# Kernel optimization log

Hardware: AMD Instinct MI355X
Metric: run time of the kernel (lower is better)

Reference implementation:

```python
import jax, jax.numpy as jnp
from jax import lax
import numpy as np

B, IMG_H, IMG_W = 8, 256, 512
NUM_CLASSES, P = 20, 32
SCALE, TOPK, IOU_THR = 32.0, 100, 0.5


def conv2d(x, w, b, stride=1, pad=1):
    y = lax.conv_general_dilated(x, w, (stride, stride), [(pad, pad), (pad, pad)],
                                 dimension_numbers=('NCHW', 'OIHW', 'NCHW'))
    return y + b[None, :, None, None]


def bilinear_resize(img, out_h, out_w):
    # img: [..., H, W]; torch F.interpolate(mode='bilinear', align_corners=False)
    H, W = img.shape[-2], img.shape[-1]
    def idx_w(n_in, n_out):
        src = (jnp.arange(n_out, dtype=jnp.float32) + 0.5) * (n_in / n_out) - 0.5
        src = jnp.clip(src, 0.0, n_in - 1)
        i0 = jnp.floor(src).astype(jnp.int32)
        i1 = jnp.minimum(i0 + 1, n_in - 1)
        return i0, i1, src - i0.astype(jnp.float32)
    y0, y1, wy = idx_w(H, out_h)
    x0, x1, wx = idx_w(W, out_w)
    top = img[..., y0, :] * (1.0 - wy)[:, None] + img[..., y1, :] * wy[:, None]
    return top[..., x0] * (1.0 - wx) + top[..., x1] * wx


def generate_anchors(fh, fw):
    ys = (jnp.arange(fh, dtype=jnp.float32) + 0.5) * (IMG_H / fh)
    xs = (jnp.arange(fw, dtype=jnp.float32) + 0.5) * (IMG_W / fw)
    cy, cx = jnp.meshgrid(ys, xs, indexing='ij')
    h = SCALE / 2
    return jnp.stack([cx - h, cy - h, cx + h, cy + h], -1).reshape(-1, 4)


def delta_to_boxes(anchors, deltas):
    a_c = (anchors[:, :2] + anchors[:, 2:]) / 2
    a_wh = anchors[:, 2:] - anchors[:, :2]
    pc = a_c + deltas[..., :2] * a_wh
    pwh = a_wh * jnp.exp(deltas[..., 2:])
    return jnp.concatenate([pc - pwh / 2, pc + pwh / 2], -1)


def nms_single(boxes, scores, labels):
    # torchvision batched_nms: offset boxes per label, greedy NMS, return kept idxs
    N = boxes.shape[0]
    off = labels.astype(boxes.dtype) * (jnp.max(boxes) + 1.0)
    b = boxes + off[:, None]
    order = jnp.argsort(-scores)
    bs = b[order]
    area = (bs[:, 2] - bs[:, 0]) * (bs[:, 3] - bs[:, 1])
    lt = jnp.maximum(bs[:, None, :2], bs[None, :, :2])
    rb = jnp.minimum(bs[:, None, 2:], bs[None, :, 2:])
    wh = jnp.clip(rb - lt, 0.0)
    inter = wh[..., 0] * wh[..., 1]
    iou = inter / (area[:, None] + area[None, :] - inter + 1e-9)
    idxs = jnp.arange(N)
    def body(i, suppressed):
        keep_i = jnp.logical_not(suppressed[i])
        row = (iou[i] > IOU_THR) & (idxs > i)
        return jnp.where(keep_i, suppressed | row, suppressed)
    suppressed = lax.fori_loop(0, N, body, jnp.zeros(N, bool))
    keep_mask = ~suppressed
    rank = jnp.cumsum(keep_mask) - 1
    slots = jnp.where(keep_mask & (rank < TOPK), rank, TOPK)
    out = jnp.full(TOPK + 1, -1, jnp.int32).at[slots].set(order.astype(jnp.int32))
    return out[:TOPK]


def setup_inputs():
    key = jax.random.key(0)
    ks = jax.random.split(key, 17)
    def cw(k, o, i, kh, kw_):
        return jax.random.normal(k, (o, i, kh, kw_), jnp.float32) / np.sqrt(i * kh * kw_)
    return {
        'images': jax.random.normal(ks[0], (B, 3, IMG_H, IMG_W), jnp.float32),
        'w1': cw(ks[1], 64, 3, 3, 3),   'b1': jnp.zeros(64, jnp.float32),
        'w2': cw(ks[2], 128, 64, 3, 3), 'b2': jnp.zeros(128, jnp.float32),
        'w3': cw(ks[3], 256, 128, 3, 3),'b3': jnp.zeros(256, jnp.float32),
        'pw1': cw(ks[4], 256, 256, 3, 3), 'pb1': jnp.zeros(256, jnp.float32),
        'pw2': cw(ks[5], P, 256, 1, 1),   'pb2': jnp.zeros(P, jnp.float32),
        'cw_': cw(ks[6], NUM_CLASSES + 1, 256, 3, 3), 'cb': jnp.zeros(NUM_CLASSES + 1, jnp.float32),
        'bw': cw(ks[7], 4, 256, 3, 3),  'bb': jnp.zeros(4, jnp.float32),
        'kw': cw(ks[8], P, 256, 3, 3),  'kb': jnp.zeros(P, jnp.float32),
    }


def reference(images, w1, b1, w2, b2, w3, b3, pw1, pb1, pw2, pb2, cw_, cb, bw, bb, kw, kb):
    x = jax.nn.relu(conv2d(images, w1, b1, stride=2))
    x = jax.nn.relu(conv2d(x, w2, b2, stride=2))
    feat = jax.nn.relu(conv2d(x, w3, b3, stride=2))          # [B,256,32,64]
    proto = conv2d(jax.nn.relu(conv2d(feat, pw1, pb1)), pw2, pb2, pad=0)  # [B,P,32,64]
    fh, fw = feat.shape[2], feat.shape[3]
    def head(w, b, c):
        return conv2d(feat, w, b).transpose(0, 2, 3, 1).reshape(B, -1, c)
    cls = head(cw_, cb, NUM_CLASSES + 1)     # [B,N,C+1]
    box = head(bw, bb, 4)                    # [B,N,4]
    coef = head(kw, kb, P)                   # [B,N,P]
    anchors = generate_anchors(fh, fw)       # [N,4]
    probs = jax.nn.softmax(cls, -1)[..., :-1]
    scores = probs.max(-1)
    labels = probs.argmax(-1).astype(jnp.int32)
    boxes = delta_to_boxes(anchors, box)     # [B,N,4]
    keep = jax.vmap(nms_single)(boxes, scores, labels)   # [B,100], -1 pad
    valid = keep >= 0
    ki = jnp.clip(keep, 0)
    take = lambda a: jnp.take_along_axis(a, ki[..., None] if a.ndim == 3 else ki, axis=1)
    boxes_k = take(boxes) * valid[..., None]
    scores_k = take(scores) * valid
    labels_k = jnp.where(valid, take(labels), 0)
    coef_k = jnp.take_along_axis(coef, ki[..., None], axis=1)   # [B,100,P]
    m = jax.nn.sigmoid(jnp.einsum('bkp,bphw->bkhw', coef_k, proto))
    masks = bilinear_resize(m, IMG_H, IMG_W) > 0.5
    masks = masks & valid[..., None, None]
    return boxes_k, scores_k, labels_k, masks, valid
```

## Files before the change

kernel.cpp:

```cpp
#include <hip/hip_runtime.h>
#include <hip/hip_bf16.h>
#include <math.h>

#define BB 8
#define NCLS 21
#define NANCH 2048
#define TOPK_N 100

static const size_t OFF_X1HI = 0;
static const size_t OFF_X1LO = 34344960;
static const size_t OFF_X2HI = 68689920;
static const size_t OFF_X2LO = 86261760;
static const size_t OFF_FTHI = 103833600;
static const size_t OFF_FTLO = 113025024;
static const size_t OFF_WT1  = 122216448;
static const size_t OFF_A2H  = 122223616;
static const size_t OFF_A2L  = 122371072;
static const size_t OFF_A3H  = 122518528;
static const size_t OFF_A3L  = 123108352;
static const size_t OFF_AHH  = 123698176;
static const size_t OFF_AHL  = 123993088;
static const size_t OFF_AP1H = 124288000;
static const size_t OFF_AP1L = 125467648;
static const size_t OFF_WTP2 = 126647296;
static const size_t OFF_BH   = 126680064;
static const size_t OFF_HOUT = 126680576;
static const size_t OFF_P1   = 130874880;
static const size_t OFF_PROTO= 147652096;
static const size_t OFF_BOXES= 149749248;
static const size_t OFF_SCORES=150011392;
static const size_t OFF_LABELS=150076928;
static const size_t OFF_ORDER= 150142464;
static const size_t OFF_SB   = 150208000;
static const size_t OFF_IOU  = 150470144;
static const size_t OFF_KEEP = 154664448;
static const size_t OFF_MAXB = 154668032;

static const size_t OUT_BOXES  = 0;
static const size_t OUT_SCORES = 3200;
static const size_t OUT_LABELS = 4000;
static const size_t OUT_MASKS  = 4800;
static const size_t OUT_VALID  = 104862400;

typedef __attribute__((ext_vector_type(8))) short bf16x8;
typedef __attribute__((ext_vector_type(4))) float f32x4;

__device__ __forceinline__ unsigned encf(float f){
  unsigned u = __float_as_uint(f);
  return (u & 0x80000000u) ? ~u : (u | 0x80000000u);
}
__device__ __forceinline__ float decf(unsigned u){
  unsigned b = (u & 0x80000000u) ? (u & 0x7fffffffu) : ~u;
  return __uint_as_float(b);
}
__device__ __forceinline__ short f2bf(float f){
  __hip_bfloat16 h = __float2bfloat16(f);
  return *(short*)&h;
}
__device__ __forceinline__ float bf2f(short h){
  return __uint_as_float(((unsigned)(unsigned short)h) << 16);
}

__global__ void halok3(short* __restrict__ x1hi, short* __restrict__ x1lo,
                       short* __restrict__ x2hi, short* __restrict__ x2lo,
                       short* __restrict__ fthi, short* __restrict__ ftlo,
                       unsigned* __restrict__ maxb){
  int i = blockIdx.x*256 + threadIdx.x;
  if (i < BB) maxb[i] = 0u;
  short *hi, *lo; int Hp, Wp, cell, bg;
  if (i < 49408){
    hi=x1hi; lo=x1lo; Hp=130; Wp=258; cell = i % 772; bg = i / 772;
  } else if (i < 99072){
    int j = i - 49408; hi=x2hi; lo=x2lo; Hp=66; Wp=130; cell = j % 388; bg = j / 388;
  } else if (i < 149248){
    int j = i - 99072; hi=fthi; lo=ftlo; Hp=34; Wp=66; cell = j % 196; bg = j / 196;
  } else return;
  int y, x;
  if (cell < Wp)        { y = 0;      x = cell; }
  else if (cell < 2*Wp) { y = Hp-1;   x = cell - Wp; }
  else { int r = cell - 2*Wp; y = 1 + (r>>1); x = (r&1) ? (Wp-1) : 0; }
  size_t ad = (((size_t)bg*Hp + y)*Wp + x)*8;
  bf16x8 z = (bf16x8){0,0,0,0,0,0,0,0};
  *(bf16x8*)(hi + ad) = z;
  *(bf16x8*)(lo + ad) = z;
}

template<int CIN,int COUT,int KK>
__device__ __forceinline__ void packw_body(int i, const float* __restrict__ w,
                                           float* __restrict__ wT){
  if (i >= CIN*KK*COUT) return;
  int co = i % COUT; int r = i / COUT;
  int ci = r / KK,  k = r % KK;
  wT[i] = w[(co*CIN + ci)*KK + k];
}

template<int CIN,int COUT>
__device__ __forceinline__ void packA_body(int i, const float* __restrict__ w,
                                           short* __restrict__ Ahi, short* __restrict__ Alo){
  constexpr int K = CIN*9;
  constexpr int KS = K/32;
  if (i >= COUT*K) return;
  int sub  = i & 7;
  int lane = (i >> 3) & 63;
  int rest = i >> 9;
  int ks = rest % KS;
  int mt = rest / KS;
  int m = mt*16 + (lane & 15);
  int k = ks*32 + (lane >> 4)*8 + sub;
  int tap = k / CIN, ci = k - tap*CIN;
  float v = w[(m*CIN + ci)*9 + tap];
  short h = f2bf(v);
  Ahi[i] = h;
  Alo[i] = f2bf(v - bf2f(h));
}

__device__ __forceinline__ void packAh_body(int i,
    const float* __restrict__ cw, const float* __restrict__ bw,
    const float* __restrict__ kw, const float* __restrict__ cb,
    const float* __restrict__ bb, const float* __restrict__ kb,
    short* __restrict__ Ahi, short* __restrict__ Alo, float* __restrict__ bh){
  if (i < 64){
    float v = 0.f;
    if (i < 21) v = cb[i]; else if (i < 25) v = bb[i-21]; else if (i < 57) v = kb[i-25];
    bh[i] = v;
  }
  if (i >= 64*2304) return;
  constexpr int KS = 72;
  int sub  = i & 7;
  int lane = (i >> 3) & 63;
  int rest = i >> 9;
  int ks = rest % KS;
  int mt = rest / KS;
  int m = mt*16 + (lane & 15);
  int k = ks*32 + (lane >> 4)*8 + sub;
  int tap = k >> 8, ci = k & 255;
  float v = 0.f;
  if (m < 21)      v = cw[(m*256 + ci)*9 + tap];
  else if (m < 25) v = bw[((m-21)*256 + ci)*9 + tap];
  else if (m < 57) v = kw[((m-25)*256 + ci)*9 + tap];
  short h = f2bf(v);
  Ahi[i] = h;
  Alo[i] = f2bf(v - bf2f(h));
}

__global__ void packall(const float* __restrict__ w1, float* __restrict__ wT1,
                        const float* __restrict__ w2, short* __restrict__ a2h, short* __restrict__ a2l,
                        const float* __restrict__ w3, short* __restrict__ a3h, short* __restrict__ a3l,
                        const float* __restrict__ pw1, short* __restrict__ ap1h, short* __restrict__ ap1l,
                        const float* __restrict__ cw, const float* __restrict__ bw,
                        const float* __restrict__ kw, const float* __restrict__ cb,
                        const float* __restrict__ bb, const float* __restrict__ kb,
                        short* __restrict__ ahh, short* __restrict__ ahl, float* __restrict__ bh,
                        const float* __restrict__ pw2, float* __restrict__ wTp2){
  int blk = blockIdx.x, t = threadIdx.x;
  if (blk < 288)        packA_body<64,128>(blk*256+t, w2, a2h, a2l);
  else if (blk < 1440)  packA_body<128,256>((blk-288)*256+t, w3, a3h, a3l);
  else if (blk < 3744)  packA_body<256,256>((blk-1440)*256+t, pw1, ap1h, ap1l);
  else if (blk < 4320)  packAh_body((blk-3744)*256+t, cw,bw,kw,cb,bb,kb, ahh,ahl,bh);
  else if (blk < 4327)  packw_body<3,64,9>((blk-4320)*256+t, w1, wT1);
  else                  packw_body<256,32,1>((blk-4327)*256+t, pw2, wTp2);
}

__global__ __launch_bounds__(256) void conv1k(const float* __restrict__ img,
    const float* __restrict__ wT, const float* __restrict__ bias,
    short* __restrict__ x1hi, short* __restrict__ x1lo){
  const int b   = blockIdx.z;
  const int co0 = blockIdx.y * 16;
  const int g   = blockIdx.x*256 + threadIdx.x;
  const int y  = g >> 7;
  const int x0 = (g & 127) << 1;

  float acc[16][2];
#pragma unroll
  for (int c=0;c<16;c++){
    float bv = bias[co0+c];
    acc[c][0] = bv; acc[c][1] = bv;
  }
  int   off[3][5];
  float msk[3][5];
#pragma unroll
  for (int kh=0;kh<3;kh++){
    int iy = y*2 - 1 + kh;
    bool okr = (iy >= 0) && (iy < 256);
    int ro = okr ? iy*512 : 0;
#pragma unroll
    for (int t=0;t<5;t++){
      int col = x0*2 - 1 + t;
      bool ok = okr && (col >= 0) && (col < 512);
      off[kh][t] = ok ? (ro + col) : 0;
      msk[kh][t] = ok ? 1.f : 0.f;
    }
  }
  const float* inb = img + (size_t)b*3*256*512;
  for (int ci=0; ci<3; ci++){
    const float* inc = inb + (size_t)ci*256*512;
    float v[3][5];
#pragma unroll
    for (int kh=0;kh<3;kh++)
#pragma unroll
      for (int t=0;t<5;t++)
        v[kh][t] = inc[off[kh][t]] * msk[kh][t];
    const float* wp = wT + ci*9*64 + co0;
#pragma unroll
    for (int kh=0;kh<3;kh++)
#pragma unroll
    for (int kw=0;kw<3;kw++){
      const float* wq = wp + (kh*3+kw)*64;
#pragma unroll
      for (int c=0;c<16;c++){
        float wv = wq[c];
        acc[c][0] = fmaf(wv, v[kh][2*0+kw], acc[c][0]);
        acc[c][1] = fmaf(wv, v[kh][2*1+kw], acc[c][1]);
      }
    }
  }
#pragma unroll
  for (int s=0;s<2;s++){
    short hv[16] __attribute__((aligned(16)));
    short lv[16] __attribute__((aligned(16)));
#pragma unroll
    for (int c=0;c<16;c++){
      float r = fmaxf(acc[c][s], 0.f);
      short h = f2bf(r);
      hv[c] = h;
      lv[c] = f2bf(r - bf2f(h));
    }
#pragma unroll
    for (int g2=0; g2<2; g2++){
      size_t ad = (((size_t)(b*8 + (co0>>3) + g2)*130 + (y+1))*258 + (x0+s+1))*8;
      *(bf16x8*)(x1hi + ad) = *(bf16x8*)(hv + g2*8);
      *(bf16x8*)(x1lo + ad) = *(bf16x8*)(lv + g2*8);
    }
  }
}

template<int CIN,int K,int M,int MW,int NW,int S,int IPH,int IPW,int NXB,
         bool SPLIT,bool STAGELO,bool STAGEREG,int EMODE,int OPH,int OPW>
__global__ __launch_bounds__(NW*64) void cgemm_row(
    const short* __restrict__ Ahi, const short* __restrict__ Alo,
    const short* __restrict__ Bhi, const short* __restrict__ Blo,
    const float* __restrict__ bias, float* __restrict__ outf,
    short* __restrict__ outhi, short* __restrict__ outlo){
  static_assert(CIN % 32 == 0, "CIN must be multiple of 32");
  constexpr int NT = 64*32;
  constexpr int KS = K/32;
  constexpr int CG = CIN/8;
  constexpr int SW  = 64*S + 2;
  constexpr int SWP = (S==2) ? (SW/2 + 1) : SW;
  constexpr int PARS = (S==2) ? 2 : 1;
  constexpr int LOOFF = CG*PARS*SWP*8;
  constexpr int BUFS = (SPLIT && STAGELO) ? 2 : 1;
  constexpr int NTH = NW*64;
  constexpr int NLD = (CG*SW + NTH - 1)/NTH;
  __shared__ __align__(16) short sB[BUFS*LOOFF];

  const int b    = blockIdx.z;
  const int oy   = blockIdx.x / NXB;
  const int xb   = (blockIdx.x % NXB) * 64;
  const int wave = threadIdx.x >> 6;
  const int lane = threadIdx.x & 63;
  const int lm = lane & 15, lq = lane >> 4;
  const int m0 = (blockIdx.y * NW + wave) * (MW*16);
  const int tid = threadIdx.x;

  f32x4 acc[MW][4];
#pragma unroll
  for (int i=0;i<MW;i++)
#pragma unroll
    for (int j=0;j<4;j++) acc[i][j] = (f32x4){0.f,0.f,0.f,0.f};

  const short* Ah_l = Ahi + (size_t)lane*8;
  const short* Al_l = Alo + (size_t)lane*8;
  const int mt0 = m0 >> 4;
  const size_t plane = (size_t)IPH*IPW;
  const short* Bl0 = Blo + ((size_t)b*CG + lq)*plane*8;

  bf16x8 rh[STAGEREG ? NLD : 1];
  bf16x8 rl[(STAGEREG && SPLIT && STAGELO) ? NLD : 1];

  auto LOADS = [&](int iyv){
    const short* srch = Bhi + (((size_t)b*CG*IPH + iyv)*IPW + (size_t)(xb*S))*8;
#pragma unroll
    for (int t=0;t<NLD;t++){
      int c = tid + t*NTH;
      if (c < CG*SW){
        int g = c / SW, p = c - g*SW;
        rh[t] = *(const bf16x8*)(srch + ((size_t)g*plane + p)*8);
      }
    }
    if constexpr (SPLIT && STAGELO){
      const short* srcl = Blo + (((size_t)b*CG*IPH + iyv)*IPW + (size_t)(xb*S))*8;
#pragma unroll
      for (int t=0;t<NLD;t++){
        int c = tid + t*NTH;
        if (c < CG*SW){
          int g = c / SW, p = c - g*SW;
          rl[t] = *(const bf16x8*)(srcl + ((size_t)g*plane + p)*8);
        }
      }
    }
  };
  auto WRITES = [&](){
#pragma unroll
    for (int t=0;t<NLD;t++){
      int c = tid + t*NTH;
      if (c < CG*SW){
        int g = c / SW, p = c - g*SW;
        int dst = (S==2) ? ((g*2 + (p&1))*SWP + (p>>1)) : (g*SW + p);
        *(bf16x8*)(&sB[(size_t)dst*8]) = rh[t];
        if constexpr (SPLIT && STAGELO)
          *(bf16x8*)(&sB[LOOFF + (size_t)dst*8]) = rl[t];
      }
    }
  };

  if constexpr (STAGEREG){
    LOADS(oy*S);
    WRITES();
    __syncthreads();
  }

#pragma unroll 1
  for (int dy=0; dy<3; dy++){
    const int iy = oy*S + dy;
    if constexpr (STAGEREG){
      if (dy < 2) LOADS(oy*S + dy + 1);
    } else {
      __syncthreads();
      {
        const short* srch = Bhi + (((size_t)b*CG*IPH + iy)*IPW + (size_t)(xb*S))*8;
        for (int c = tid; c < CG*SW; c += NTH){
          int g = c / SW, p = c - g*SW;
          int dst = (S==2) ? ((g*2 + (p&1))*SWP + (p>>1)) : (g*SW + p);
          *(bf16x8*)(&sB[(size_t)dst*8]) =
            *(const bf16x8*)(srch + ((size_t)g*plane + p)*8);
        }
        if constexpr (SPLIT && STAGELO){
          const short* srcl = Blo + (((size_t)b*CG*IPH + iy)*IPW + (size_t)(xb*S))*8;
          for (int c = tid; c < CG*SW; c += NTH){
            int g = c / SW, p = c - g*SW;
            int dst = (S==2) ? ((g*2 + (p&1))*SWP + (p>>1)) : (g*SW + p);
            *(bf16x8*)(&sB[LOOFF + (size_t)dst*8]) =
              *(const bf16x8*)(srcl + ((size_t)g*plane + p)*8);
          }
        }
      }
      __syncthreads();
    }
#pragma unroll
    for (int dx=0; dx<3; dx++){
      const int tap = dy*3 + dx;
      const int ksb = tap*(CIN/32);
#pragma unroll
      for (int kc=0; kc<CIN; kc+=32){
        const int ks = ksb + (kc>>5);
        int ra[4];
#pragma unroll
        for (int j=0;j<4;j++){
          int pc = (j*16 + lm)*S + dx;
          ra[j] = (S==2) ? ((((kc>>3) + lq)*2 + (pc&1))*SWP + (pc>>1))
                         : (((kc>>3) + lq)*SW + pc);
        }
        bf16x8 ah[MW], bh_[4];
#pragma unroll
        for (int i=0;i<MW;i++)
          ah[i] = *(const bf16x8*)(Ah_l + ((size_t)(mt0+i)*KS + ks)*512);
#pragma unroll
        for (int j=0;j<4;j++)
          bh_[j] = *(const bf16x8*)(&sB[(size_t)ra[j]*8]);
        if constexpr (SPLIT){
          bf16x8 al[MW], bl_[4];
#pragma unroll
          for (int i=0;i<MW;i++)
            al[i] = *(const bf16x8*)(Al_l + ((size_t)(mt0+i)*KS + ks)*512);
          if constexpr (STAGELO){
#pragma unroll
            for (int j=0;j<4;j++)
              bl_[j] = *(const bf16x8*)(&sB[LOOFF + (size_t)ra[j]*8]);
          } else {
#pragma unroll
            for (int j=0;j<4;j++){
              size_t pix = (size_t)iy*IPW + (size_t)((xb + j*16 + lm)*S + dx);
              bl_[j] = *(const bf16x8*)(Bl0 + ((size_t)(kc>>3)*plane + pix)*8);
            }
          }
#pragma unroll
          for (int j=0;j<4;j++)
#pragma unroll
            for (int i=0;i<MW;i++)
              acc[i][j] = __builtin_amdgcn_mfma_f32_16x16x32_bf16(ah[i], bh_[j], acc[i][j], 0,0,0);
#pragma unroll
          for (int j=0;j<4;j++)
#pragma unroll
            for (int i=0;i<MW;i++)
              acc[i][j] = __builtin_amdgcn_mfma_f32_16x16x32_bf16(ah[i], bl_[j], acc[i][j], 0,0,0);
#pragma unroll
          for (int j=0;j<4;j++)
#pragma unroll
            for (int i=0;i<MW;i++)
              acc[i][j] = __builtin_amdgcn_mfma_f32_16x16x32_bf16(al[i], bh_[j], acc[i][j], 0,0,0);
        } else {
#pragma unroll
          for (int j=0;j<4;j++)
#pragma unroll
            for (int i=0;i<MW;i++)
              acc[i][j] = __builtin_amdgcn_mfma_f32_16x16x32_bf16(ah[i], bh_[j], acc[i][j], 0,0,0);
        }
      }
    }
    if constexpr (STAGEREG){
      if (dy < 2){
        __syncthreads();
        WRITES();
        __syncthreads();
      }
    }
  }

#pragma unroll
  for (int i=0;i<MW;i++){
#pragma unroll
    for (int r=0;r<4;r++){
      const int m = m0 + i*16 + lq*4 + r;
      const float bv = bias[m];
      if constexpr (EMODE == 0){
#pragma unroll
        for (int j=0;j<4;j++){
          const int ox = xb + j*16 + lm;
          float v = fmaxf(acc[i][j][r] + bv, 0.f);
          short h = f2bf(v);
          short l = f2bf(v - bf2f(h));
          size_t ad = ((((size_t)(b*(M/8) + (m>>3))*OPH + (oy+1))*OPW + (ox+1)))*8 + (m&7);
          outhi[ad] = h;
          outlo[ad] = l;
        }
      } else {
        float* cp = outf + ((size_t)b*M + m)*NT + oy*64 + lm;
#pragma unroll
        for (int j=0;j<4;j++){
          float v = acc[i][j][r] + bv;
          if constexpr (EMODE == 2) v = fmaxf(v, 0.f);
          cp[j*16] = v;
        }
      }
    }
  }
}

__global__ __launch_bounds__(256) void headsdec(
    const short* __restrict__ Ahi, const short* __restrict__ Alo,
    const short* __restrict__ Bhi, const short* __restrict__ Blo,
    const float* __restrict__ bias, float* __restrict__ hout,
    float* __restrict__ boxes, float* __restrict__ scores,
    int* __restrict__ labels, unsigned* __restrict__ maxb){
  constexpr int KS = 72;
  constexpr int CG = 32;
  constexpr int SW = 66;
  constexpr int IPH = 34, IPW = 66;
  constexpr int LOOFF = CG*SW*8;
  constexpr int NLD = (CG*SW + 255)/256;
  __shared__ __align__(16) short sB[2*LOOFF];

  const int b  = blockIdx.z;
  const int oy = blockIdx.x;
  const int wave = threadIdx.x >> 6;
  const int lane = threadIdx.x & 63;
  const int lm = lane & 15, lq = lane >> 4;
  const int tid = threadIdx.x;

  f32x4 acc[4];
#pragma unroll
  for (int j=0;j<4;j++) acc[j] = (f32x4){0.f,0.f,0.f,0.f};

  const short* Ah_l = Ahi + (size_t)lane*8;
  const short* Al_l = Alo + (size_t)lane*8;
  const size_t plane = (size_t)IPH*IPW;

  bf16x8 rh[NLD], rl[NLD];
  auto HLOADS = [&](int iyv){
    const short* srch = Bhi + ((size_t)b*CG*IPH + iyv)*IPW*8;
    const short* srcl = Blo + ((size_t)b*CG*IPH + iyv)*IPW*8;
#pragma unroll
    for (int t=0;t<NLD;t++){
      int c = tid + t*256;
      if (c < CG*SW){
        int g = c / SW, p = c - g*SW;
        rh[t] = *(const bf16x8*)(srch + ((size_t)g*plane + p)*8);
        rl[t] = *(const bf16x8*)(srcl + ((size_t)g*plane + p)*8);
      }
    }
  };
  auto HWRITES = [&](){
#pragma unroll
    for (int t=0;t<NLD;t++){
      int c = tid + t*256;
      if (c < CG*SW){
        *(bf16x8*)(&sB[(size_t)c*8]) = rh[t];
        *(bf16x8*)(&sB[LOOFF + (size_t)c*8]) = rl[t];
      }
    }
  };

  HLOADS(oy);
  HWRITES();
  __syncthreads();

#pragma unroll 1
  for (int dy=0; dy<3; dy++){
    if (dy < 2) HLOADS(oy + dy + 1);
#pragma unroll
    for (int dx=0; dx<3; dx++){
      const int tap = dy*3 + dx;
      const int ksb = tap*8;
#pragma unroll
      for (int kc=0; kc<256; kc+=32){
        const int ks = ksb + (kc>>5);
        int ra[4];
#pragma unroll
        for (int j=0;j<4;j++) ra[j] = ((kc>>3) + lq)*SW + (j*16 + lm) + dx;
        bf16x8 bh_[4], bl_[4];
#pragma unroll
        for (int j=0;j<4;j++){
          bh_[j] = *(const bf16x8*)(&sB[(size_t)ra[j]*8]);
          bl_[j] = *(const bf16x8*)(&sB[LOOFF + (size_t)ra[j]*8]);
        }
        bf16x8 ah = *(const bf16x8*)(Ah_l + ((size_t)wave*KS + ks)*512);
        bf16x8 al = *(const bf16x8*)(Al_l + ((size_t)wave*KS + ks)*512);
#pragma unroll
        for (int j=0;j<4;j++)
          acc[j] = __builtin_amdgcn_mfma_f32_16x16x32_bf16(ah, bh_[j], acc[j], 0,0,0);
#pragma unroll
        for (int j=0;j<4;j++)
          acc[j] = __builtin_amdgcn_mfma_f32_16x16x32_bf16(ah, bl_[j], acc[j], 0,0,0);
#pragma unroll
        for (int j=0;j<4;j++)
          acc[j] = __builtin_amdgcn_mfma_f32_16x16x32_bf16(al, bh_[j], acc[j], 0,0,0);
      }
    }
    if (dy < 2){
      __syncthreads();
      HWRITES();
      __syncthreads();
    }
  }

  __syncthreads();
  float* sF = (float*)sB;
#pragma unroll
  for (int r=0;r<4;r++){
    const int m = wave*16 + lq*4 + r;
    const float bv = bias[m];
    float* cp = hout + ((size_t)b*64 + m)*NANCH + oy*64 + lm;
#pragma unroll
    for (int j=0;j<4;j++){
      float v = acc[j][r] + bv;
      cp[j*16] = v;
      sF[m*68 + j*16 + lm] = v;
    }
  }
  __syncthreads();

  if (tid < 64){
    const int n = oy*64 + tid;
    float l[NCLS];
    float M = -1e30f;
#pragma unroll
    for (int c=0;c<NCLS;c++){ l[c] = sF[c*68 + tid]; M = fmaxf(M, l[c]); }
    float denom = 0.f;
#pragma unroll
    for (int c=0;c<NCLS;c++) denom += expf(l[c]-M);
    float best = -1.f; int bi = 0;
#pragma unroll
    for (int c=0;c<NCLS-1;c++){
      float e = expf(l[c]-M);
      if (e > best){ best = e; bi = c; }
    }
    scores[(size_t)b*NANCH + n] = best/denom;
    labels[(size_t)b*NANCH + n] = bi;

    float dxv = sF[21*68 + tid], dyv = sF[22*68 + tid];
    float dwv = sF[23*68 + tid], dhv = sF[24*68 + tid];
    const int yy = n >> 6, xx = n & 63;
    float cx = (xx+0.5f)*8.f, cy = (yy+0.5f)*8.f;
    float px = cx + dxv*32.f, py = cy + dyv*32.f;
    float pw = 32.f*expf(dwv), ph = 32.f*expf(dhv);
    float x1 = px - 0.5f*pw, y1 = py - 0.5f*ph;
    float x2 = px + 0.5f*pw, y2 = py + 0.5f*ph;
    float* bo = boxes + ((size_t)b*NANCH + n)*4;
    bo[0]=x1; bo[1]=y1; bo[2]=x2; bo[3]=y2;
    float mx = fmaxf(fmaxf(x1,y1), fmaxf(x2,y2));
#pragma unroll
    for (int off=32; off>0; off>>=1) mx = fmaxf(mx, __shfl_down(mx, off));
    if (tid == 0) atomicMax(maxb + b, encf(mx));
  }
}

__global__ __launch_bounds__(256) void pw2k2(const float* __restrict__ p1,
    const float* __restrict__ wT, const float* __restrict__ bias,
    float* __restrict__ proto){
  const int b  = blockIdx.y;
  const int sp = blockIdx.x*256 + threadIdx.x;
  float acc[32];
#pragma unroll
  for (int c=0;c<32;c++) acc[c] = bias[c];
  const float* pb = p1 + (size_t)b*256*NANCH + sp;
  for (int ci=0;ci<256;ci++){
    float v = pb[(size_t)ci*NANCH];
    const float* wq = wT + ci*32;
#pragma unroll
    for (int c=0;c<32;c++) acc[c] = fmaf(v, wq[c], acc[c]);
  }
#pragma unroll
  for (int c=0;c<32;c++)
    proto[((size_t)b*32 + c)*NANCH + sp] = acc[c];
}

__global__ void __launch_bounds__(1024) sortk(const float* __restrict__ scores,
                     const float* __restrict__ boxes, const int* __restrict__ labels,
                     const unsigned* __restrict__ maxb,
                     int* __restrict__ order, float* __restrict__ sb){
  __shared__ float sc[NANCH];
  __shared__ int   id[NANCH];
  const int b = blockIdx.x, t = threadIdx.x;
  for (int i=t;i<NANCH;i+=1024){ sc[i]=scores[(size_t)b*NANCH+i]; id[i]=i; }
  __syncthreads();
  for (int k=2;k<=NANCH;k<<=1){
    for (int j=k>>1;j>0;j>>=1){
      for (int i=t;i<NANCH;i+=1024){
        int ixj = i ^ j;
        if (ixj > i){
          float sa=sc[i], sb_=sc[ixj]; int ia=id[i], ib=id[ixj];
          bool dir = ((i & k) == 0);
          bool before_ba = (sb_ > sa) || (sb_ == sa && ib < ia);
          if (before_ba == dir){ sc[i]=sb_; sc[ixj]=sa; id[i]=ib; id[ixj]=ia; }
        }
      }
      __syncthreads();
    }
  }
  float mboff = decf(maxb[b]) + 1.0f;
  for (int r=t;r<NANCH;r+=1024){
    int o = id[r];
    order[(size_t)b*NANCH + r] = o;
    float off = (float)labels[(size_t)b*NANCH + o] * mboff;
    const float* bo = boxes + ((size_t)b*NANCH + o)*4;
    float* sp = sb + ((size_t)b*NANCH + r)*4;
    sp[0]=bo[0]+off; sp[1]=bo[1]+off; sp[2]=bo[2]+off; sp[3]=bo[3]+off;
  }
}

__global__ void ioumask(const float* __restrict__ sb, unsigned long long* __restrict__ iou){
  const int b = blockIdx.y;
  const int gid = blockIdx.x*blockDim.x + threadIdx.x;
  const int i = gid >> 5, w = gid & 31;
  const float* base = sb + (size_t)b*NANCH*4;
  unsigned long long bits = 0ull;
  const int j0 = w << 6;
  if (j0 + 63 > i){
    float x1=base[i*4], y1=base[i*4+1], x2=base[i*4+2], y2=base[i*4+3];
    float ai = (x2-x1)*(y2-y1);
    for (int jj=0;jj<64;jj++){
      int j = j0 + jj;
      if (j > i){
        float bx1=base[j*4], by1=base[j*4+1], bx2=base[j*4+2], by2=base[j*4+3];
        float lx=fmaxf(x1,bx1), ly=fmaxf(y1,by1);
        float rx=fminf(x2,bx2), ry=fminf(y2,by2);
        float ww=fmaxf(rx-lx,0.f), hh=fmaxf(ry-ly,0.f);
        float inter = ww*hh;
        float aj = (bx2-bx1)*(by2-by1);
        float v = inter/(ai + aj - inter + 1e-9f);
        if (v > 0.5f) bits |= (1ull << jj);
      }
    }
  }
  iou[((size_t)b*NANCH + i)*32 + w] = bits;
}

__global__ void nmsgather(const unsigned long long* __restrict__ iou,
                          const int* __restrict__ order,
                          const float* __restrict__ boxes, const float* __restrict__ scores,
                          const int* __restrict__ labels,
                          int* __restrict__ keep, float* __restrict__ out){
  const int b = blockIdx.x, lane = threadIdx.x;
  __shared__ int s_keep[TOPK_N];
  unsigned long long sup = 0ull;
  int k = 0, i = 0;
  while (k < TOPK_N){
    unsigned long long avail = (lane < 32) ? ~sup : 0ull;
    const int wi = i >> 6;
    if (lane < wi) avail = 0ull;
    else if (lane == wi) avail &= (~0ull) << (i & 63);
    unsigned long long ball = __ballot(avail != 0ull);
    if (!ball) break;
    int w0 = (int)__builtin_ctzll(ball);
    unsigned long long aw = __shfl(avail, w0);
    int b0 = (int)__builtin_ctzll(aw);
    i = (w0 << 6) + b0;
    int ov = order[(size_t)b*NANCH + i];
    if (lane == 0) s_keep[k] = ov;
    k++;
    unsigned long long row = (lane < 32) ? iou[((size_t)b*NANCH + i)*32 + lane] : 0ull;
    sup |= row;
    i++;
    if (i >= NANCH) break;
  }
  __syncthreads();
  for (int r = lane; r < TOPK_N; r += 64){
    int kv = (r < k) ? s_keep[r] : -1;
    keep[b*TOPK_N + r] = kv;
    float valid = (kv >= 0) ? 1.f : 0.f;
    int kc = (kv < 0) ? 0 : kv;
    const float* bo = boxes + ((size_t)b*NANCH + kc)*4;
#pragma unroll
    for (int c=0;c<4;c++) out[OUT_BOXES + ((size_t)b*TOPK_N + r)*4 + c] = bo[c]*valid;
    out[OUT_SCORES + b*TOPK_N + r] = scores[(size_t)b*NANCH + kc]*valid;
    out[OUT_LABELS + b*TOPK_N + r] = (kv >= 0) ? (float)labels[(size_t)b*NANCH + kc] : 0.f;
    out[OUT_VALID  + b*TOPK_N + r] = valid;
  }
}

__global__ __launch_bounds__(256) void maskresize(const int* __restrict__ keep,
    const float* __restrict__ hout, const float* __restrict__ proto,
    float* __restrict__ out){
  const int b = blockIdx.y, r = blockIdx.x;
  float* obase = out + OUT_MASKS + ((size_t)b*TOPK_N + r)*131072;
  int ki = keep[b*TOPK_N + r];
  if (ki < 0){
    float4 z = make_float4(0.f,0.f,0.f,0.f);
    for (int idx = threadIdx.x; idx < 32768; idx += 256)
      ((float4*)obase)[idx] = z;
    return;
  }
  __shared__ float cf[32];
  __shared__ float sm[NANCH];
  if (threadIdx.x < 32)
    cf[threadIdx.x] = hout[((size_t)b*64 + 25 + threadIdx.x)*NANCH + ki];
  __syncthreads();
  for (int s = threadIdx.x; s < NANCH; s += 256){
    float acc = 0.f;
#pragma unroll
    for (int p=0;p<32;p++) acc = fmaf(cf[p], proto[((size_t)b*32 + p)*NANCH + s], acc);
    sm[s] = 1.f/(1.f + expf(-acc));
  }
  __syncthreads();
  for (int pid = threadIdx.x; pid < 32768; pid += 256){
    const int y  = pid >> 7;
    const int x4 = (pid & 127) << 2;
    float sy = (y + 0.5f)*0.125f - 0.5f;
    sy = fminf(fmaxf(sy, 0.f), 31.f);
    int y0 = (int)floorf(sy);
    int y1 = min(y0+1, 31);
    float wy = sy - (float)y0;
    const float* r0 = sm + y0*64;
    const float* r1 = sm + y1*64;
    float res[4];
#pragma unroll
    for (int kk=0;kk<4;kk++){
      int x = x4 + kk;
      float sx = (x + 0.5f)*0.125f - 0.5f;
      sx = fminf(fmaxf(sx, 0.f), 63.f);
      int x0 = (int)floorf(sx);
      int x1 = min(x0+1, 63);
      float wx = sx - (float)x0;
      float t0 = r0[x0]*(1.f-wy) + r1[x0]*wy;
      float t1 = r0[x1]*(1.f-wy) + r1[x1]*wy;
      float v  = t0*(1.f-wx) + t1*wx;
      res[kk] = (v > 0.5f) ? 1.f : 0.f;
    }
    *(float4*)(obase + y*512 + x4) = make_float4(res[0], res[1], res[2], res[3]);
  }
}

extern "C" void kernel_launch(void* const* d_in, const int* in_sizes, int n_in,
                              void* d_out, int out_size, void* d_ws, size_t ws_size,
                              hipStream_t stream) {
  const float* images=(const float*)d_in[0];
  const float* w1=(const float*)d_in[1];  const float* b1=(const float*)d_in[2];
  const float* w2=(const float*)d_in[3];  const float* b2=(const float*)d_in[4];
  const float* w3=(const float*)d_in[5];  const float* b3=(const float*)d_in[6];
  const float* pw1=(const float*)d_in[7]; const float* pb1=(const float*)d_in[8];
  const float* pw2=(const float*)d_in[9]; const float* pb2=(const float*)d_in[10];
  const float* cw=(const float*)d_in[11]; const float* cb=(const float*)d_in[12];
  const float* bw=(const float*)d_in[13]; const float* bb=(const float*)d_in[14];
  const float* kw=(const float*)d_in[15]; const float* kb=(const float*)d_in[16];
  float* out = (float*)d_out;
  char* ws = (char*)d_ws;

  short* x1hi = (short*)(ws + OFF_X1HI);
  short* x1lo = (short*)(ws + OFF_X1LO);
  short* x2hi = (short*)(ws + OFF_X2HI);
  short* x2lo = (short*)(ws + OFF_X2LO);
  short* fthi = (short*)(ws + OFF_FTHI);
  short* ftlo = (short*)(ws + OFF_FTLO);
  float* wT1  = (float*)(ws + OFF_WT1);
  short* a2h  = (short*)(ws + OFF_A2H);
  short* a2l  = (short*)(ws + OFF_A2L);
  short* a3h  = (short*)(ws + OFF_A3H);
  short* a3l  = (short*)(ws + OFF_A3L);
  short* ahh  = (short*)(ws + OFF_AHH);
  short* ahl  = (short*)(ws + OFF_AHL);
  short* ap1h = (short*)(ws + OFF_AP1H);
  short* ap1l = (short*)(ws + OFF_AP1L);
  float* wTp2 = (float*)(ws + OFF_WTP2);
  float* bh   = (float*)(ws + OFF_BH);
  float* hout = (float*)(ws + OFF_HOUT);
  float* p1   = (float*)(ws + OFF_P1);
  float* proto= (float*)(ws + OFF_PROTO);
  float* boxes= (float*)(ws + OFF_BOXES);
  float* scores=(float*)(ws + OFF_SCORES);
  int*   labels=(int*)  (ws + OFF_LABELS);
  int*   order =(int*)  (ws + OFF_ORDER);
  float* sb   = (float*)(ws + OFF_SB);
  unsigned long long* iou = (unsigned long long*)(ws + OFF_IOU);
  int*   keep = (int*)  (ws + OFF_KEEP);
  unsigned* maxb = (unsigned*)(ws + OFF_MAXB);

  halok3<<<dim3(583), 256, 0, stream>>>(x1hi, x1lo, x2hi, x2lo, fthi, ftlo, maxb);

  packall<<<dim3(4359), 256, 0, stream>>>(w1, wT1, w2, a2h, a2l, w3, a3h, a3l,
                                          pw1, ap1h, ap1l, cw, bw, kw, cb, bb, kb,
                                          ahh, ahl, bh, pw2, wTp2);

  conv1k<<<dim3(64,4,BB), 256, 0, stream>>>(images, wT1, b1, x1hi, x1lo);

  cgemm_row<64,576,128,2,4,2,130,258,2,true,true,false,0,66,130>
      <<<dim3(128,1,BB), 256, 0, stream>>>(a2h, a2l, x1hi, x1lo, b2, nullptr, x2hi, x2lo);

  cgemm_row<128,1152,256,2,4,2,66,130,1,true,true,true,0,34,66>
      <<<dim3(32,2,BB), 256, 0, stream>>>(a3h, a3l, x2hi, x2lo, b3, nullptr, fthi, ftlo);

  headsdec<<<dim3(32,1,BB), 256, 0, stream>>>(ahh, ahl, fthi, ftlo, bh, hout,
                                              boxes, scores, labels, maxb);

  cgemm_row<256,2304,256,2,4,1,34,66,1,false,false,true,2,1,1>
      <<<dim3(32,2,BB), 256, 0, stream>>>(ap1h, ap1l, fthi, fthi, pb1, p1, nullptr, nullptr);

  pw2k2<<<dim3(8,BB), 256, 0, stream>>>(p1, wTp2, pb2, proto);

  sortk<<<dim3(BB), 1024, 0, stream>>>(scores, boxes, labels, maxb, order, sb);
  ioumask<<<dim3(256,BB), 256, 0, stream>>>(sb, iou);
  nmsgather<<<dim3(BB), 64, 0, stream>>>(iou, order, boxes, scores, labels, keep, out);

  maskresize<<<dim3(TOPK_N,BB), 256, 0, stream>>>(keep, hout, proto, out);
}
```

Baseline: 953.4 us.

## Merge prep, head/pw1, and pw2/sort kernels into combined launches

Halo zeroing, weight packing and conv1 now run as blocks of a single megaprep launch, with conv1 weights transposed into shared memory so the separate wT1 pack is dropped. The heads/decode kernel and the proto pw1 GEMM become branches of one launch that share a shared-memory buffer. The pw2 projection and the per-image sort share another launch. The layer-2 GEMM template also switches STAGEREG on. The aim is to cut launch count and let independent work run side by side. The risk is that conv1 blocks in megaprep read the packed weights' neighbours without ordering, since packing and conv1 have no dependency, and that the fused kernels take on larger shared-memory and register footprints, which lowers occupancy.

```diff
diff --git a/kernel.cpp b/kernel.cpp
--- a/kernel.cpp
+++ b/kernel.cpp
@@ -61,30 +61,6 @@
   return __uint_as_float(((unsigned)(unsigned short)h) << 16);
 }
 
-__global__ void halok3(short* __restrict__ x1hi, short* __restrict__ x1lo,
-                       short* __restrict__ x2hi, short* __restrict__ x2lo,
-                       short* __restrict__ fthi, short* __restrict__ ftlo,
-                       unsigned* __restrict__ maxb){
-  int i = blockIdx.x*256 + threadIdx.x;
-  if (i < BB) maxb[i] = 0u;
-  short *hi, *lo; int Hp, Wp, cell, bg;
-  if (i < 49408){
-    hi=x1hi; lo=x1lo; Hp=130; Wp=258; cell = i % 772; bg = i / 772;
-  } else if (i < 99072){
-    int j = i - 49408; hi=x2hi; lo=x2lo; Hp=66; Wp=130; cell = j % 388; bg = j / 388;
-  } else if (i < 149248){
-    int j = i - 99072; hi=fthi; lo=ftlo; Hp=34; Wp=66; cell = j % 196; bg = j / 196;
-  } else return;
-  int y, x;
-  if (cell < Wp)        { y = 0;      x = cell; }
-  else if (cell < 2*Wp) { y = Hp-1;   x = cell - Wp; }
-  else { int r = cell - 2*Wp; y = 1 + (r>>1); x = (r&1) ? (Wp-1) : 0; }
-  size_t ad = (((size_t)bg*Hp + y)*Wp + x)*8;
-  bf16x8 z = (bf16x8){0,0,0,0,0,0,0,0};
-  *(bf16x8*)(hi + ad) = z;
-  *(bf16x8*)(lo + ad) = z;
-}
-
 template<int CIN,int COUT,int KK>
 __device__ __forceinline__ void packw_body(int i, const float* __restrict__ w,
                                            float* __restrict__ wT){
@@ -143,37 +119,71 @@
   Alo[i] = f2bf(v - bf2f(h));
 }
 
-__global__ void packall(const float* __restrict__ w1, float* __restrict__ wT1,
-                        const float* __restrict__ w2, short* __restrict__ a2h, short* __restrict__ a2l,
-                        const float* __restrict__ w3, short* __restrict__ a3h, short* __restrict__ a3l,
-                        const float* __restrict__ pw1, short* __restrict__ ap1h, short* __restrict__ ap1l,
-                        const float* __restrict__ cw, const float* __restrict__ bw,
-                        const float* __restrict__ kw, const float* __restrict__ cb,
-                        const float* __restrict__ bb, const float* __restrict__ kb,
-                        short* __restrict__ ahh, short* __restrict__ ahl, float* __restrict__ bh,
-                        const float* __restrict__ pw2, float* __restrict__ wTp2){
-  int blk = blockIdx.x, t = threadIdx.x;
-  if (blk < 288)        packA_body<64,128>(blk*256+t, w2, a2h, a2l);
-  else if (blk < 1440)  packA_body<128,256>((blk-288)*256+t, w3, a3h, a3l);
-  else if (blk < 3744)  packA_body<256,256>((blk-1440)*256+t, pw1, ap1h, ap1l);
-  else if (blk < 4320)  packAh_body((blk-3744)*256+t, cw,bw,kw,cb,bb,kb, ahh,ahl,bh);
-  else if (blk < 4327)  packw_body<3,64,9>((blk-4320)*256+t, w1, wT1);
-  else                  packw_body<256,32,1>((blk-4327)*256+t, pw2, wTp2);
-}
-
-__global__ __launch_bounds__(256) void conv1k(const float* __restrict__ img,
-    const float* __restrict__ wT, const float* __restrict__ bias,
-    short* __restrict__ x1hi, short* __restrict__ x1lo){
-  const int b   = blockIdx.z;
-  const int co0 = blockIdx.y * 16;
-  const int g   = blockIdx.x*256 + threadIdx.x;
+__global__ __launch_bounds__(256) void megaprep(
+    const float* __restrict__ images, const float* __restrict__ w1, const float* __restrict__ b1,
+    const float* __restrict__ w2, short* __restrict__ a2h, short* __restrict__ a2l,
+    const float* __restrict__ w3, short* __restrict__ a3h, short* __restrict__ a3l,
+    const float* __restrict__ pw1, short* __restrict__ ap1h, short* __restrict__ ap1l,
+    const float* __restrict__ cw, const float* __restrict__ bw, const float* __restrict__ kw,
+    const float* __restrict__ cb, const float* __restrict__ bb, const float* __restrict__ kb,
+    short* __restrict__ ahh, short* __restrict__ ahl, float* __restrict__ bh,
+    const float* __restrict__ pw2, float* __restrict__ wTp2,
+    short* __restrict__ x1hi, short* __restrict__ x1lo,
+    short* __restrict__ x2hi, short* __restrict__ x2lo,
+    short* __restrict__ fthi, short* __restrict__ ftlo,
+    unsigned* __restrict__ maxb){
+  __shared__ float sw[27*64];
+  const int blk = blockIdx.x, tid = threadIdx.x;
+
+  if (blk < 583){
+    int i = blk*256 + tid;
+    if (i < BB) maxb[i] = 0u;
+    short *hi, *lo; int Hp, Wp, cell, bg;
+    if (i < 49408){
+      hi=x1hi; lo=x1lo; Hp=130; Wp=258; cell = i % 772; bg = i / 772;
+    } else if (i < 99072){
+      int j = i - 49408; hi=x2hi; lo=x2lo; Hp=66; Wp=130; cell = j % 388; bg = j / 388;
+    } else if (i < 149248){
+      int j = i - 99072; hi=fthi; lo=ftlo; Hp=34; Wp=66; cell = j % 196; bg = j / 196;
+    } else return;
+    int y, x;
+    if (cell < Wp)        { y = 0;      x = cell; }
+    else if (cell < 2*Wp) { y = Hp-1;   x = cell - Wp; }
+    else { int r = cell - 2*Wp; y = 1 + (r>>1); x = (r&1) ? (Wp-1) : 0; }
+    size_t ad = (((size_t)bg*Hp + y)*Wp + x)*8;
+    bf16x8 z = (bf16x8){0,0,0,0,0,0,0,0};
+    *(bf16x8*)(hi + ad) = z;
+    *(bf16x8*)(lo + ad) = z;
+    return;
+  }
+  if (blk < 4935){
+    int lb = blk - 583;
+    if (lb < 288)        packA_body<64,128>(lb*256+tid, w2, a2h, a2l);
+    else if (lb < 1440)  packA_body<128,256>((lb-288)*256+tid, w3, a3h, a3l);
+    else if (lb < 3744)  packA_body<256,256>((lb-1440)*256+tid, pw1, ap1h, ap1l);
+    else if (lb < 4320)  packAh_body((lb-3744)*256+tid, cw,bw,kw,cb,bb,kb, ahh,ahl,bh);
+    else                 packw_body<256,32,1>((lb-4320)*256+tid, pw2, wTp2);
+    return;
+  }
+
+  const int cblk = blk - 4935;
+  const int bxc = cblk & 63;
+  const int co0 = ((cblk >> 6) & 3) * 16;
+  const int b   = cblk >> 8;
+  for (int idx = tid; idx < 1728; idx += 256){
+    int r = idx >> 6, co = idx & 63;
+    sw[idx] = w1[co*27 + r];
+  }
+  __syncthreads();
+
+  const int g  = bxc*256 + tid;
   const int y  = g >> 7;
   const int x0 = (g & 127) << 1;
 
   float acc[16][2];
 #pragma unroll
   for (int c=0;c<16;c++){
-    float bv = bias[co0+c];
+    float bv = b1[co0+c];
     acc[c][0] = bv; acc[c][1] = bv;
   }
   int   off[3][5];
@@ -191,7 +201,7 @@
       msk[kh][t] = ok ? 1.f : 0.f;
     }
   }
-  const float* inb = img + (size_t)b*3*256*512;
+  const float* inb = images + (size_t)b*3*256*512;
   for (int ci=0; ci<3; ci++){
     const float* inc = inb + (size_t)ci*256*512;
     float v[3][5];
@@ -200,17 +210,17 @@
 #pragma unroll
       for (int t=0;t<5;t++)
         v[kh][t] = inc[off[kh][t]] * msk[kh][t];
-    const float* wp = wT + ci*9*64 + co0;
+    const float* wp = sw + ci*9*64 + co0;
 #pragma unroll
     for (int kh=0;kh<3;kh++)
 #pragma unroll
-    for (int kw=0;kw<3;kw++){
-      const float* wq = wp + (kh*3+kw)*64;
+    for (int kw2=0;kw2<3;kw2++){
+      const float* wq = wp + (kh*3+kw2)*64;
 #pragma unroll
       for (int c=0;c<16;c++){
         float wv = wq[c];
-        acc[c][0] = fmaf(wv, v[kh][2*0+kw], acc[c][0]);
-        acc[c][1] = fmaf(wv, v[kh][2*1+kw], acc[c][1]);
+        acc[c][0] = fmaf(wv, v[kh][2*0+kw2], acc[c][0]);
+        acc[c][1] = fmaf(wv, v[kh][2*1+kw2], acc[c][1]);
       }
     }
   }
@@ -236,7 +246,8 @@
 
 template<int CIN,int K,int M,int MW,int NW,int S,int IPH,int IPW,int NXB,
          bool SPLIT,bool STAGELO,bool STAGEREG,int EMODE,int OPH,int OPW>
-__global__ __launch_bounds__(NW*64) void cgemm_row(
+__device__ __forceinline__ void cgemm_row_body(
+    short* sB, int bxi, int byi, int bzi,
     const short* __restrict__ Ahi, const short* __restrict__ Alo,
     const short* __restrict__ Bhi, const short* __restrict__ Blo,
     const float* __restrict__ bias, float* __restrict__ outf,
@@ -247,20 +258,17 @@
   constexpr int CG = CIN/8;
   constexpr int SW  = 64*S + 2;
   constexpr int SWP = (S==2) ? (SW/2 + 1) : SW;
-  constexpr int PARS = (S==2) ? 2 : 1;
-  constexpr int LOOFF = CG*PARS*SWP*8;
-  constexpr int BUFS = (SPLIT && STAGELO) ? 2 : 1;
+  constexpr int LOOFF = CG*((S==2)?2:1)*SWP*8;
   constexpr int NTH = NW*64;
   constexpr int NLD = (CG*SW + NTH - 1)/NTH;
-  __shared__ __align__(16) short sB[BUFS*LOOFF];
-
-  const int b    = blockIdx.z;
-  const int oy   = blockIdx.x / NXB;
-  const int xb   = (blockIdx.x % NXB) * 64;
+
+  const int b    = bzi;
+  const int oy   = bxi / NXB;
+  const int xb   = (bxi % NXB) * 64;
   const int wave = threadIdx.x >> 6;
   const int lane = threadIdx.x & 63;
   const int lm = lane & 15, lq = lane >> 4;
-  const int m0 = (blockIdx.y * NW + wave) * (MW*16);
+  const int m0 = (byi * NW + wave) * (MW*16);
   const int tid = threadIdx.x;
 
   f32x4 acc[MW][4];
@@ -447,7 +455,26 @@
   }
 }
 
-__global__ __launch_bounds__(256) void headsdec(
+template<int CIN,int K,int M,int MW,int NW,int S,int IPH,int IPW,int NXB,
+         bool SPLIT,bool STAGELO,bool STAGEREG,int EMODE,int OPH,int OPW>
+__global__ __launch_bounds__(NW*64) void cgemm_row(
+    const short* __restrict__ Ahi, const short* __restrict__ Alo,
+    const short* __restrict__ Bhi, const short* __restrict__ Blo,
+    const float* __restrict__ bias, float* __restrict__ outf,
+    short* __restrict__ outhi, short* __restrict__ outlo){
+  constexpr int CG = CIN/8;
+  constexpr int SW  = 64*S + 2;
+  constexpr int SWP = (S==2) ? (SW/2 + 1) : SW;
+  constexpr int LOOFF = CG*((S==2)?2:1)*SWP*8;
+  constexpr int BUFS = (SPLIT && STAGELO) ? 2 : 1;
+  __shared__ __align__(16) short sB[BUFS*LOOFF];
+  cgemm_row_body<CIN,K,M,MW,NW,S,IPH,IPW,NXB,SPLIT,STAGELO,STAGEREG,EMODE,OPH,OPW>(
+      sB, blockIdx.x, blockIdx.y, blockIdx.z,
+      Ahi, Alo, Bhi, Blo, bias, outf, outhi, outlo);
+}
+
+__device__ __forceinline__ void headsdec_body(
+    short* sB, int oy, int b,
     const short* __restrict__ Ahi, const short* __restrict__ Alo,
     const short* __restrict__ Bhi, const short* __restrict__ Blo,
     const float* __restrict__ bias, float* __restrict__ hout,
@@ -459,10 +486,7 @@
   constexpr int IPH = 34, IPW = 66;
   constexpr int LOOFF = CG*SW*8;
   constexpr int NLD = (CG*SW + 255)/256;
-  __shared__ __align__(16) short sB[2*LOOFF];
-
-  const int b  = blockIdx.z;
-  const int oy = blockIdx.x;
+
   const int wave = threadIdx.x >> 6;
   const int lane = threadIdx.x & 63;
   const int lm = lane & 15, lq = lane >> 4;
@@ -595,33 +619,54 @@
   }
 }
 
-__global__ __launch_bounds__(256) void pw2k2(const float* __restrict__ p1,
-    const float* __restrict__ wT, const float* __restrict__ bias,
-    float* __restrict__ proto){
-  const int b  = blockIdx.y;
-  const int sp = blockIdx.x*256 + threadIdx.x;
-  float acc[32];
-#pragma unroll
-  for (int c=0;c<32;c++) acc[c] = bias[c];
-  const float* pb = p1 + (size_t)b*256*NANCH + sp;
-  for (int ci=0;ci<256;ci++){
-    float v = pb[(size_t)ci*NANCH];
-    const float* wq = wT + ci*32;
-#pragma unroll
-    for (int c=0;c<32;c++) acc[c] = fmaf(v, wq[c], acc[c]);
-  }
-#pragma unroll
-  for (int c=0;c<32;c++)
-    proto[((size_t)b*32 + c)*NANCH + sp] = acc[c];
-}
-
-__global__ void __launch_bounds__(1024) sortk(const float* __restrict__ scores,
-                     const float* __restrict__ boxes, const int* __restrict__ labels,
-                     const unsigned* __restrict__ maxb,
-                     int* __restrict__ order, float* __restrict__ sb){
+__global__ __launch_bounds__(256) void headpw1k(
+    const short* __restrict__ ahh, const short* __restrict__ ahl,
+    const short* __restrict__ ap1h,
+    const short* __restrict__ fthi, const short* __restrict__ ftlo,
+    const float* __restrict__ bh, const float* __restrict__ pb1,
+    float* __restrict__ hout, float* __restrict__ p1,
+    float* __restrict__ boxes, float* __restrict__ scores,
+    int* __restrict__ labels, unsigned* __restrict__ maxb){
+  __shared__ __align__(16) short smem[33792];
+  const int bx = blockIdx.x, b = blockIdx.z;
+  if (bx < 32){
+    headsdec_body(smem, bx, b, ahh, ahl, fthi, ftlo, bh, hout,
+                  boxes, scores, labels, maxb);
+  } else {
+    const int lx = bx - 32;
+    cgemm_row_body<256,2304,256,2,4,1,34,66,1,false,false,true,2,1,1>(
+        smem, lx & 31, lx >> 5, b, ap1h, ap1h, fthi, fthi, pb1, p1, nullptr, nullptr);
+  }
+}
+
+__global__ void __launch_bounds__(1024) pw2sortk(
+    const float* __restrict__ p1, const float* __restrict__ wT,
+    const float* __restrict__ biasp, float* __restrict__ proto,
+    const float* __restrict__ scores, const float* __restrict__ boxes,
+    const int* __restrict__ labels, const unsigned* __restrict__ maxb,
+    int* __restrict__ order, float* __restrict__ sb){
   __shared__ float sc[NANCH];
   __shared__ int   id[NANCH];
-  const int b = blockIdx.x, t = threadIdx.x;
+  const int bx = blockIdx.x, t = threadIdx.x;
+  if (bx < 16){
+    const int b  = bx >> 1;
+    const int sp = (bx & 1)*1024 + t;
+    float acc[32];
+#pragma unroll
+    for (int c=0;c<32;c++) acc[c] = biasp[c];
+    const float* pb = p1 + (size_t)b*256*NANCH + sp;
+    for (int ci=0;ci<256;ci++){
+      float v = pb[(size_t)ci*NANCH];
+      const float* wq = wT + ci*32;
+#pragma unroll
+      for (int c=0;c<32;c++) acc[c] = fmaf(v, wq[c], acc[c]);
+    }
+#pragma unroll
+    for (int c=0;c<32;c++)
+      proto[((size_t)b*32 + c)*NANCH + sp] = acc[c];
+    return;
+  }
+  const int b = bx - 16;
   for (int i=t;i<NANCH;i+=1024){ sc[i]=scores[(size_t)b*NANCH+i]; id[i]=i; }
   __syncthreads();
   for (int k=2;k<=NANCH;k<<=1){
@@ -792,7 +837,6 @@
   short* x2lo = (short*)(ws + OFF_X2LO);
   short* fthi = (short*)(ws + OFF_FTHI);
   short* ftlo = (short*)(ws + OFF_FTLO);
-  float* wT1  = (float*)(ws + OFF_WT1);
   short* a2h  = (short*)(ws + OFF_A2H);
   short* a2l  = (short*)(ws + OFF_A2L);
   short* a3h  = (short*)(ws + OFF_A3H);
@@ -815,29 +859,24 @@
   int*   keep = (int*)  (ws + OFF_KEEP);
   unsigned* maxb = (unsigned*)(ws + OFF_MAXB);
 
-  halok3<<<dim3(583), 256, 0, stream>>>(x1hi, x1lo, x2hi, x2lo, fthi, ftlo, maxb);
-
-  packall<<<dim3(4359), 256, 0, stream>>>(w1, wT1, w2, a2h, a2l, w3, a3h, a3l,
-                                          pw1, ap1h, ap1l, cw, bw, kw, cb, bb, kb,
-                                          ahh, ahl, bh, pw2, wTp2);
-
-  conv1k<<<dim3(64,4,BB), 256, 0, stream>>>(images, wT1, b1, x1hi, x1lo);
-
-  cgemm_row<64,576,128,2,4,2,130,258,2,true,true,false,0,66,130>
+  megaprep<<<dim3(6983), 256, 0, stream>>>(
+      images, w1, b1, w2, a2h, a2l, w3, a3h, a3l, pw1, ap1h, ap1l,
+      cw, bw, kw, cb, bb, kb, ahh, ahl, bh, pw2, wTp2,
+      x1hi, x1lo, x2hi, x2lo, fthi, ftlo, maxb);
+
+  cgemm_row<64,576,128,2,4,2,130,258,2,true,true,true,0,66,130>
       <<<dim3(128,1,BB), 256, 0, stream>>>(a2h, a2l, x1hi, x1lo, b2, nullptr, x2hi, x2lo);
 
   cgemm_row<128,1152,256,2,4,2,66,130,1,true,true,true,0,34,66>
       <<<dim3(32,2,BB), 256, 0, stream>>>(a3h, a3l, x2hi, x2lo, b3, nullptr, fthi, ftlo);
 
-  headsdec<<<dim3(32,1,BB), 256, 0, stream>>>(ahh, ahl, fthi, ftlo, bh, hout,
+  headpw1k<<<dim3(96,1,BB), 256, 0, stream>>>(ahh, ahl, ap1h, fthi, ftlo,
+                                              bh, pb1, hout, p1,
                                               boxes, scores, labels, maxb);
 
-  cgemm_row<256,2304,256,2,4,1,34,66,1,false,false,true,2,1,1>
-      <<<dim3(32,2,BB), 256, 0, stream>>>(ap1h, ap1l, fthi, fthi, pb1, p1, nullptr, nullptr);
-
-  pw2k2<<<dim3(8,BB), 256, 0, stream>>>(p1, wTp2, pb2, proto);
-
-  sortk<<<dim3(BB), 1024, 0, stream>>>(scores, boxes, labels, maxb, order, sb);
+  pw2sortk<<<dim3(24), 1024, 0, stream>>>(p1, wTp2, pb2, proto,
+                                          scores, boxes, labels, maxb, order, sb);
+
   ioumask<<<dim3(256,BB), 256, 0, stream>>>(sb, iou);
   nmsgather<<<dim3(BB), 64, 0, stream>>>(iou, order, boxes, scores, labels, keep, out);
 
```

After: 889.4 us. 1.07x faster.
